# Kernel optimization log

Hardware: AMD Instinct MI355X
Metric: run time of the kernel (lower is better)

## Reference

```python
import jax, jax.numpy as jnp
import numpy as np

TWO_PI = 2.0 * np.pi
POW25_7 = 25.0 ** 7
M_RGB2XYZ = np.array([[0.4124564, 0.3575761, 0.1804375],
                      [0.2126729, 0.7151522, 0.072175],
                      [0.0193339, 0.119192, 0.9503041]], dtype=np.float32)
XYZ_REF = np.array([0.95047, 1.0, 1.08883], dtype=np.float32)


def rgb_to_lab(rgb):
    # rgb: [B, 3] in [0, 1]
    lin = jnp.where(rgb > 0.04045, ((rgb + 0.055) / 1.055) ** 2.4, rgb / 12.92)
    xyz = lin @ jnp.asarray(M_RGB2XYZ).T
    xyz_n = xyz / jnp.asarray(XYZ_REF)
    f = jnp.where(xyz_n > 0.008856, jnp.cbrt(xyz_n), 7.787 * xyz_n + 16.0 / 116.0)
    L = 116.0 * f[:, 1] - 16.0
    a = 500.0 * (f[:, 0] - f[:, 1])
    b = 200.0 * (f[:, 1] - f[:, 2])
    return L, a, b


def delta_e_2000(lab1, lab2):
    L1, a1, b1 = lab1
    L2, a2, b2 = lab2
    C1 = jnp.sqrt(a1 ** 2 + b1 ** 2)
    C2 = jnp.sqrt(a2 ** 2 + b2 ** 2)
    C_avg = (C1 + C2) / 2
    C_avg7 = C_avg ** 7
    G = 0.5 * (1 - jnp.sqrt(C_avg7 / (C_avg7 + POW25_7)))
    a1p = a1 * (1 + G)
    a2p = a2 * (1 + G)
    C1p = jnp.sqrt(a1p ** 2 + b1 ** 2)
    C2p = jnp.sqrt(a2p ** 2 + b2 ** 2)
    h1p = jnp.arctan2(b1, a1p) % TWO_PI
    h2p = jnp.arctan2(b2, a2p) % TWO_PI
    dL = L2 - L1
    dC = C2p - C1p
    dh = h2p - h1p
    dh = jnp.where(jnp.abs(dh) > np.pi,
                   jnp.where(h2p <= h1p, dh + TWO_PI, dh - TWO_PI), dh)
    dH = 2 * jnp.sqrt(C1p * C2p) * jnp.sin(dh / 2)
    L_avg = (L1 + L2) / 2
    Cp_avg = (C1p + C2p) / 2
    h_avg = jnp.where(jnp.abs(h1p - h2p) > np.pi,
                      (h1p + h2p + TWO_PI) / 2, (h1p + h2p) / 2)
    T = (1 - 0.17 * jnp.cos(h_avg - np.pi / 6)
         + 0.24 * jnp.cos(2 * h_avg)
         + 0.32 * jnp.cos(3 * h_avg + np.pi / 30)
         - 0.2 * jnp.cos(4 * h_avg - 7 * np.pi / 20))
    theta = 30 * jnp.exp(-(((h_avg * 180.0 / np.pi) - 275.0) / 25.0) ** 2)
    Cp_avg7 = Cp_avg ** 7
    RC = 2 * jnp.sqrt(Cp_avg7 / (Cp_avg7 + POW25_7))
    RT = -jnp.sin(2 * theta) * RC
    SL = 1 + 0.015 * (L_avg - 50) ** 2 / jnp.sqrt(20 + (L_avg - 50) ** 2)
    SC = 1 + 0.045 * Cp_avg
    SH = 1 + 0.015 * Cp_avg * T
    return jnp.sqrt((dL / SL) ** 2 + (dC / SC) ** 2 + (dH / SH) ** 2
                    + RT * (dC / SC) * (dH / SH))


def setup_inputs() -> dict:
    key = jax.random.key(0)
    k1, k2 = jax.random.split(key)
    B = 16777216
    pred = jax.random.uniform(k1, (B, 3), dtype=jnp.float32)
    target = jax.random.uniform(k2, (B, 3), dtype=jnp.float32)
    return {"pred": pred, "target": target}


def reference(pred, target):
    mse_loss = jnp.mean((pred - target) ** 2, axis=1)  # [B]
    de = delta_e_2000(rgb_to_lab(pred), rgb_to_lab(target))  # [B]
    # original detaches delta_e (computed on CPU numpy, written into a new tensor)
    combined = 0.2 * mse_loss + 0.8 * jax.lax.stop_gradient(de)
    return jnp.mean(combined)
```

## Files before the change

### kernel.cpp

```cpp
#include <hip/hip_runtime.h>
#include <math.h>

#define TPB 256
#define MAXBLOCKS 8192

typedef float v4f __attribute__((ext_vector_type(4)));

__device__ __forceinline__ float fsqrt_(float x){ return __builtin_amdgcn_sqrtf(x); }
__device__ __forceinline__ float frcp_ (float x){ return __builtin_amdgcn_rcpf(x); }
__device__ __forceinline__ float frsq_ (float x){ return __builtin_amdgcn_rsqf(x); }
__device__ __forceinline__ float flog2_(float x){ return __builtin_amdgcn_logf(x); }
__device__ __forceinline__ float fexp2_(float x){ return __builtin_amdgcn_exp2f(x); }
__device__ __forceinline__ float fsinr_(float x){ return __builtin_amdgcn_sinf(x); }

__device__ __forceinline__ v4f vs(float x){ return (v4f){x, x, x, x}; }

#define V4APPLY(fn, a) ((v4f){ fn((a).x), fn((a).y), fn((a).z), fn((a).w) })
__device__ __forceinline__ v4f vsqrt(v4f a){ return V4APPLY(fsqrt_, a); }
__device__ __forceinline__ v4f vrcp (v4f a){ return V4APPLY(frcp_ , a); }
__device__ __forceinline__ v4f vrsq (v4f a){ return V4APPLY(frsq_ , a); }
__device__ __forceinline__ v4f vlog2(v4f a){ return V4APPLY(flog2_, a); }
__device__ __forceinline__ v4f vexp2(v4f a){ return V4APPLY(fexp2_, a); }
__device__ __forceinline__ v4f vsinr(v4f a){ return V4APPLY(fsinr_, a); }

#if __has_builtin(__builtin_elementwise_fma)
__device__ __forceinline__ v4f vfma(v4f a, v4f b, v4f c){ return __builtin_elementwise_fma(a,b,c); }
#else
__device__ __forceinline__ v4f vfma(v4f a, v4f b, v4f c){ return a*b + c; }
#endif
__device__ __forceinline__ v4f vmax(v4f a, v4f b){ return __builtin_elementwise_max(a,b); }
__device__ __forceinline__ v4f vmin(v4f a, v4f b){ return __builtin_elementwise_min(a,b); }
__device__ __forceinline__ v4f vabs(v4f a){ return __builtin_elementwise_abs(a); }
__device__ __forceinline__ v4f vselgt(v4f x, float t, v4f a, v4f b){
    v4f r;
    r.x = x.x > t ? a.x : b.x;
    r.y = x.y > t ? a.y : b.y;
    r.z = x.z > t ? a.z : b.z;
    r.w = x.w > t ? a.w : b.w;
    return r;
}
__device__ __forceinline__ v4f vcopysign(v4f m, v4f s){
    v4f r;
    r.x = copysignf(m.x, s.x);
    r.y = copysignf(m.y, s.y);
    r.z = copysignf(m.z, s.z);
    r.w = copysignf(m.w, s.w);
    return r;
}

__device__ __forceinline__ v4f srgb_lin(v4f c){
    v4f t = (c + vs(0.055f)) * vs(1.0f/1.055f);
    v4f p = vexp2(vs(2.4f) * vlog2(t));
    return vselgt(c, 0.04045f, p, c * vs(1.0f/12.92f));
}
__device__ __forceinline__ v4f lab_f(v4f t){
    v4f cb = vexp2(vs(1.0f/3.0f) * vlog2(t));
    return vselgt(t, 0.008856f, cb, vfma(vs(7.787f), t, vs(16.0f/116.0f)));
}

__device__ __forceinline__ void rgb2lab(v4f r, v4f g, v4f b, v4f& L, v4f& A, v4f& Bv){
    v4f lr = srgb_lin(r), lg = srgb_lin(g), lb = srgb_lin(b);
    v4f xn = vfma(vs(0.4339499f), lr, vfma(vs(0.3762098f), lg, vs(0.1898414f)*lb));
    v4f yn = vfma(vs(0.2126729f), lr, vfma(vs(0.7151522f), lg, vs(0.0721750f)*lb));
    v4f zn = vfma(vs(0.0177566f), lr, vfma(vs(0.1094680f), lg, vs(0.8727720f)*lb));
    v4f fx = lab_f(xn), fy = lab_f(yn), fz = lab_f(zn);
    L  = vfma(vs(116.0f), fy, vs(-16.0f));
    A  = vs(500.0f) * (fx - fy);
    Bv = vs(200.0f) * (fy - fz);
}

__device__ __forceinline__ v4f vatan2_2pi(v4f y, v4f x){
    v4f ax = vabs(x), ay = vabs(y);
    v4f mx = vmax(ax, ay), mn = vmin(ax, ay);
    v4f t = mn * vrcp(vmax(mx, vs(1e-38f)));
    v4f s = t * t;
    v4f p = vs(-0.01172120f);
    p = vfma(p, s, vs( 0.05265332f));
    p = vfma(p, s, vs(-0.11643287f));
    p = vfma(p, s, vs( 0.19354346f));
    p = vfma(p, s, vs(-0.33262347f));
    p = vfma(p, s, vs( 0.99997726f));
    p = p * t;
    v4f r = vselgt(ay - ax, 0.0f, vs(1.57079632679f) - p, p);
    r = vselgt(vs(0.0f) - x, 0.0f, vs(3.14159265359f) - r, r);
    r = vselgt(vs(0.0f) - y, 0.0f, vs(6.28318530718f) - r, r);
    return r;
}

__device__ __forceinline__ v4f row_loss(v4f pr, v4f pg, v4f pb,
                                        v4f tr, v4f tg, v4f tb){
    const float P257 = 6103515625.0f;

    v4f dr = pr - tr, dg = pg - tg, db = pb - tb;
    v4f mse = (dr*dr + dg*dg + db*db) * vs(1.0f/3.0f);

    v4f L1, a1, b1, L2, a2, b2;
    rgb2lab(pr, pg, pb, L1, a1, b1);
    rgb2lab(tr, tg, tb, L2, a2, b2);

    v4f C1 = vsqrt(vfma(a1, a1, b1*b1));
    v4f C2 = vsqrt(vfma(a2, a2, b2*b2));
    v4f Cav = vs(0.5f) * (C1 + C2);
    v4f c2v = Cav*Cav;
    v4f c7 = c2v*c2v*c2v*Cav;
    v4f gs = vsqrt(c7 * vrcp(c7 + vs(P257)));
    v4f opG = vfma(vs(-0.5f), gs, vs(1.5f));
    v4f a1p = a1 * opG;
    v4f a2p = a2 * opG;
    v4f C1p = vsqrt(vfma(a1p, a1p, b1*b1));
    v4f C2p = vsqrt(vfma(a2p, a2p, b2*b2));

    v4f dL = L2 - L1;
    v4f dC = C2p - C1p;

    v4f prod  = C1p * C2p;
    v4f dot   = vfma(a1p, a2p, b1*b2);
    v4f cross = vfma(a1p, b2, vs(0.0f) - a2p*b1);
    v4f dH = vcopysign(vsqrt(vmax(vs(2.0f)*(prod - dot), vs(0.0f))), cross);

    v4f Lav  = vs(0.5f) * (L1 + L2);
    v4f Cpav = vs(0.5f) * (C1p + C2p);

    v4f vx = vfma(a1p, C2p, a2p*C1p);
    v4f vy = vfma(b1 , C2p, b2 *C1p);
    v4f hav = vatan2_2pi(vy, vx);
    v4f inv = vrsq(vmax(vfma(vx, vx, vy*vy), vs(1e-30f)));
    v4f ch = vx * inv, sh = vy * inv;

    v4f cos2 = vfma(vs(2.0f)*ch, ch, vs(-1.0f));
    v4f sin2 = vs(2.0f) * sh * ch;
    v4f cos3 = ch * vfma(vs(2.0f), cos2, vs(-1.0f));
    v4f sin3 = sh * vfma(vs(2.0f), cos2, vs( 1.0f));
    v4f cos4 = vfma(vs(2.0f)*cos2, cos2, vs(-1.0f));
    v4f sin4 = vs(2.0f) * sin2 * cos2;
    v4f T = vs(1.0f);
    T = vfma(vs(-0.147224319f), ch,   T);
    T = vfma(vs(-0.085f),       sh,   T);
    T = vfma(vs( 0.24f),        cos2, T);
    T = vfma(vs( 0.318247006f), cos3, T);
    T = vfma(vs(-0.033449109f), sin3, T);
    T = vfma(vs(-0.090798100f), cos4, T);
    T = vfma(vs(-0.178201305f), sin4, T);

    v4f u = vfma(hav, vs(2.29183118f), vs(-11.0f));
    v4f theta = vs(30.0f) * vexp2(vs(-1.44269504f) * (u*u));

    v4f cp2 = Cpav*Cpav;
    v4f cp7 = cp2*cp2*cp2*Cpav;
    v4f RC = vs(2.0f) * vsqrt(cp7 * vrcp(cp7 + vs(P257)));
    v4f RT = vs(0.0f) - vsinr(theta * vs(0.31830988618f)) * RC;

    v4f Lm = Lav - vs(50.0f);
    v4f Lm2 = Lm * Lm;
    v4f SL = vfma(vs(0.015f) * Lm2, vrsq(vs(20.0f) + Lm2), vs(1.0f));
    v4f SC = vfma(vs(0.045f), Cpav, vs(1.0f));
    v4f SH = vfma(vs(0.015f) * Cpav, T, vs(1.0f));

    v4f t1 = dL * vrcp(SL);
    v4f t2 = dC * vrcp(SC);
    v4f t3 = dH * vrcp(SH);
    v4f arg = vfma(t1, t1, vfma(t2, t2, vfma(t3, t3, RT*t2*t3)));
    v4f de = vsqrt(vmax(arg, vs(0.0f)));

    return vfma(vs(0.2f), mse, vs(0.8f) * de);
}

__global__ void __launch_bounds__(TPB)
de_main(const float* __restrict__ pred, const float* __restrict__ tgt,
        float* __restrict__ partials, int B){
    int nvec = B >> 2;
    int gid = blockIdx.x * TPB + threadIdx.x;
    int stride = gridDim.x * TPB;
    v4f acc4 = vs(0.0f);

    for (int i = gid; i < nvec; i += stride){
        const float4* p4 = (const float4*)pred + (size_t)i * 3;
        const float4* t4 = (const float4*)tgt  + (size_t)i * 3;
        float4 pA = p4[0], pB = p4[1], pC = p4[2];
        float4 tA = t4[0], tB = t4[1], tC = t4[2];
        v4f pr = (v4f){pA.x, pA.w, pB.z, pC.y};
        v4f pg = (v4f){pA.y, pB.x, pB.w, pC.z};
        v4f pb = (v4f){pA.z, pB.y, pC.x, pC.w};
        v4f qr = (v4f){tA.x, tA.w, tB.z, tC.y};
        v4f qg = (v4f){tA.y, tB.x, tB.w, tC.z};
        v4f qb = (v4f){tA.z, tB.y, tC.x, tC.w};
        acc4 += row_loss(pr, pg, pb, qr, qg, qb);
    }
    float acc = acc4.x + acc4.y + acc4.z + acc4.w;

    int r = (nvec << 2) + gid;
    if (r < B){
        v4f pr = vs(pred[(size_t)r*3]), pg = vs(pred[(size_t)r*3+1]), pb = vs(pred[(size_t)r*3+2]);
        v4f qr = vs(tgt [(size_t)r*3]), qg = vs(tgt [(size_t)r*3+1]), qb = vs(tgt [(size_t)r*3+2]);
        acc += row_loss(pr, pg, pb, qr, qg, qb).x;
    }

    __shared__ float sdata[TPB];
    sdata[threadIdx.x] = acc;
    __syncthreads();
    #pragma unroll
    for (int s = TPB/2; s > 0; s >>= 1){
        if (threadIdx.x < s) sdata[threadIdx.x] += sdata[threadIdx.x + s];
        __syncthreads();
    }
    if (threadIdx.x == 0) partials[blockIdx.x] = sdata[0];
}

__global__ void __launch_bounds__(TPB)
de_final(const float* __restrict__ partials, int n, float* __restrict__ out, double invB){
    __shared__ double sd[TPB];
    double acc = 0.0;
    for (int i = threadIdx.x; i < n; i += TPB) acc += (double)partials[i];
    sd[threadIdx.x] = acc;
    __syncthreads();
    #pragma unroll
    for (int s = TPB/2; s > 0; s >>= 1){
        if (threadIdx.x < s) sd[threadIdx.x] += sd[threadIdx.x + s];
        __syncthreads();
    }
    if (threadIdx.x == 0) out[0] = (float)(sd[0] * invB);
}

extern "C" void kernel_launch(void* const* d_in, const int* in_sizes, int n_in,
                              void* d_out, int out_size, void* d_ws, size_t ws_size,
                              hipStream_t stream){
    const float* pred = (const float*)d_in[0];
    const float* tgt  = (const float*)d_in[1];
    int B = in_sizes[0] / 3;

    int nvec = B >> 2;
    int blocks = (nvec + TPB - 1) / TPB;
    if (blocks > MAXBLOCKS) blocks = MAXBLOCKS;
    size_t wcap = ws_size / sizeof(float);
    if (wcap > 0 && (size_t)blocks > wcap) blocks = (int)wcap;
    if (blocks < 1) blocks = 1;

    float* partials = (float*)d_ws;
    de_main <<<blocks, TPB, 0, stream>>>(pred, tgt, partials, B);
    de_final<<<1, TPB, 0, stream>>>(partials, blocks, (float*)d_out, 1.0/(double)B);
}
```

Before: 417.1 us.

## Replace sRGB gamma and Lab cube-root transcendentals with shared-memory interpolated LUTs

Each block builds two 1032-entry shared-memory tables, one for the sRGB linearisation and one for the Lab f() cube root. Per-channel log2/exp2 pairs become linear interpolation between two LDS reads, with the XYZ matrix pre-scaled so its outputs index the table directly. The change also fuses sqrt(x/(x+k)) into one rsq, replaces three reciprocals with one, and lowers the block cap from 8192 to 2048 so fewer blocks pay the table build. The cost is interpolation error, random-index LDS bank conflicts, and out-of-bounds reads if any input falls outside [0,1].

After: 426.3 us. +2.2%, slower.

```diff
diff --git a/kernel.cpp b/kernel.cpp
--- a/kernel.cpp
+++ b/kernel.cpp
@@ -2,7 +2,8 @@
 #include <math.h>
 
 #define TPB 256
-#define MAXBLOCKS 8192
+#define NBLOCKS 2048
+#define LUTN 1032
 
 typedef float v4f __attribute__((ext_vector_type(4)));
 
@@ -12,6 +13,7 @@
 __device__ __forceinline__ float flog2_(float x){ return __builtin_amdgcn_logf(x); }
 __device__ __forceinline__ float fexp2_(float x){ return __builtin_amdgcn_exp2f(x); }
 __device__ __forceinline__ float fsinr_(float x){ return __builtin_amdgcn_sinf(x); }
+__device__ __forceinline__ float ffract_(float x){ return x - floorf(x); }
 
 __device__ __forceinline__ v4f vs(float x){ return (v4f){x, x, x, x}; }
 
@@ -19,8 +21,6 @@
 __device__ __forceinline__ v4f vsqrt(v4f a){ return V4APPLY(fsqrt_, a); }
 __device__ __forceinline__ v4f vrcp (v4f a){ return V4APPLY(frcp_ , a); }
 __device__ __forceinline__ v4f vrsq (v4f a){ return V4APPLY(frsq_ , a); }
-__device__ __forceinline__ v4f vlog2(v4f a){ return V4APPLY(flog2_, a); }
-__device__ __forceinline__ v4f vexp2(v4f a){ return V4APPLY(fexp2_, a); }
 __device__ __forceinline__ v4f vsinr(v4f a){ return V4APPLY(fsinr_, a); }
 
 #if __has_builtin(__builtin_elementwise_fma)
@@ -48,22 +48,25 @@
     return r;
 }
 
-__device__ __forceinline__ v4f srgb_lin(v4f c){
-    v4f t = (c + vs(0.055f)) * vs(1.0f/1.055f);
-    v4f p = vexp2(vs(2.4f) * vlog2(t));
-    return vselgt(c, 0.04045f, p, c * vs(1.0f/12.92f));
-}
-__device__ __forceinline__ v4f lab_f(v4f t){
-    v4f cb = vexp2(vs(1.0f/3.0f) * vlog2(t));
-    return vselgt(t, 0.008856f, cb, vfma(vs(7.787f), t, vs(16.0f/116.0f)));
-}
-
-__device__ __forceinline__ void rgb2lab(v4f r, v4f g, v4f b, v4f& L, v4f& A, v4f& Bv){
-    v4f lr = srgb_lin(r), lg = srgb_lin(g), lb = srgb_lin(b);
-    v4f xn = vfma(vs(0.4339499f), lr, vfma(vs(0.3762098f), lg, vs(0.1898414f)*lb));
-    v4f yn = vfma(vs(0.2126729f), lr, vfma(vs(0.7151522f), lg, vs(0.0721750f)*lb));
-    v4f zn = vfma(vs(0.0177566f), lr, vfma(vs(0.1094680f), lg, vs(0.8727720f)*lb));
-    v4f fx = lab_f(xn), fy = lab_f(yn), fz = lab_f(zn);
+__device__ __forceinline__ float lut1(const float* __restrict__ lut, float v){
+    int i = (int)v;
+    float f = ffract_(v);
+    float a = lut[i], b = lut[i+1];
+    return fmaf(f, b - a, a);
+}
+__device__ __forceinline__ v4f vlut(const float* __restrict__ lut, v4f v){
+    return (v4f){ lut1(lut, v.x), lut1(lut, v.y), lut1(lut, v.z), lut1(lut, v.w) };
+}
+
+__device__ __forceinline__ void rgb2lab(const float* __restrict__ lutS, const float* __restrict__ lutF,
+                                        v4f r, v4f g, v4f b, v4f& L, v4f& A, v4f& Bv){
+    v4f lr = vlut(lutS, r * vs(1024.0f));
+    v4f lg = vlut(lutS, g * vs(1024.0f));
+    v4f lb = vlut(lutS, b * vs(1024.0f));
+    v4f xi = vfma(vs(444.364687f), lr, vfma(vs(385.238808f), lg, vs(194.397593f)*lb));
+    v4f yi = vfma(vs(217.777050f), lr, vfma(vs(732.315853f), lg, vs( 73.907200f)*lb));
+    v4f zi = vfma(vs( 18.182738f), lr, vfma(vs(112.095395f), lg, vs(893.719306f)*lb));
+    v4f fx = vlut(lutF, xi), fy = vlut(lutF, yi), fz = vlut(lutF, zi);
     L  = vfma(vs(116.0f), fy, vs(-16.0f));
     A  = vs(500.0f) * (fx - fy);
     Bv = vs(200.0f) * (fy - fz);
@@ -87,7 +90,8 @@
     return r;
 }
 
-__device__ __forceinline__ v4f row_loss(v4f pr, v4f pg, v4f pb,
+__device__ __forceinline__ v4f row_loss(const float* __restrict__ lutS, const float* __restrict__ lutF,
+                                        v4f pr, v4f pg, v4f pb,
                                         v4f tr, v4f tg, v4f tb){
     const float P257 = 6103515625.0f;
 
@@ -95,15 +99,15 @@
     v4f mse = (dr*dr + dg*dg + db*db) * vs(1.0f/3.0f);
 
     v4f L1, a1, b1, L2, a2, b2;
-    rgb2lab(pr, pg, pb, L1, a1, b1);
-    rgb2lab(tr, tg, tb, L2, a2, b2);
+    rgb2lab(lutS, lutF, pr, pg, pb, L1, a1, b1);
+    rgb2lab(lutS, lutF, tr, tg, tb, L2, a2, b2);
 
     v4f C1 = vsqrt(vfma(a1, a1, b1*b1));
     v4f C2 = vsqrt(vfma(a2, a2, b2*b2));
     v4f Cav = vs(0.5f) * (C1 + C2);
     v4f c2v = Cav*Cav;
     v4f c7 = c2v*c2v*c2v*Cav;
-    v4f gs = vsqrt(c7 * vrcp(c7 + vs(P257)));
+    v4f gs = c7 * vrsq(vmax(c7*(c7 + vs(P257)), vs(1e-30f)));
     v4f opG = vfma(vs(-0.5f), gs, vs(1.5f));
     v4f a1p = a1 * opG;
     v4f a2p = a2 * opG;
@@ -143,11 +147,11 @@
     T = vfma(vs(-0.178201305f), sin4, T);
 
     v4f u = vfma(hav, vs(2.29183118f), vs(-11.0f));
-    v4f theta = vs(30.0f) * vexp2(vs(-1.44269504f) * (u*u));
+    v4f theta = vs(30.0f) * V4APPLY(fexp2_, (vs(-1.44269504f) * (u*u)));
 
     v4f cp2 = Cpav*Cpav;
     v4f cp7 = cp2*cp2*cp2*Cpav;
-    v4f RC = vs(2.0f) * vsqrt(cp7 * vrcp(cp7 + vs(P257)));
+    v4f RC = vs(2.0f) * (cp7 * vrsq(vmax(cp7*(cp7 + vs(P257)), vs(1e-30f))));
     v4f RT = vs(0.0f) - vsinr(theta * vs(0.31830988618f)) * RC;
 
     v4f Lm = Lav - vs(50.0f);
@@ -156,9 +160,13 @@
     v4f SC = vfma(vs(0.045f), Cpav, vs(1.0f));
     v4f SH = vfma(vs(0.015f) * Cpav, T, vs(1.0f));
 
-    v4f t1 = dL * vrcp(SL);
-    v4f t2 = dC * vrcp(SC);
-    v4f t3 = dH * vrcp(SH);
+    v4f SCSH = SC * SH;
+    v4f SLSH = SL * SH;
+    v4f SLSC = SL * SC;
+    v4f R = vrcp(SLSC * SH);
+    v4f t1 = dL * (SCSH * R);
+    v4f t2 = dC * (SLSH * R);
+    v4f t3 = dH * (SLSC * R);
     v4f arg = vfma(t1, t1, vfma(t2, t2, vfma(t3, t3, RT*t2*t3)));
     v4f de = vsqrt(vmax(arg, vs(0.0f)));
 
@@ -168,6 +176,17 @@
 __global__ void __launch_bounds__(TPB)
 de_main(const float* __restrict__ pred, const float* __restrict__ tgt,
         float* __restrict__ partials, int B){
+    __shared__ float lutS[LUTN];
+    __shared__ float lutF[LUTN];
+    for (int i = threadIdx.x; i < LUTN; i += TPB){
+        float c = (float)i * (1.0f/1024.0f);
+        float p = fexp2_(2.4f * flog2_((c + 0.055f) * (1.0f/1.055f)));
+        lutS[i] = (c > 0.04045f) ? p : c * (1.0f/12.92f);
+        float cb = fexp2_((1.0f/3.0f) * flog2_(fmaxf(c, 1e-20f)));
+        lutF[i] = (c > 0.008856f) ? cb : fmaf(7.787f, c, 16.0f/116.0f);
+    }
+    __syncthreads();
+
     int nvec = B >> 2;
     int gid = blockIdx.x * TPB + threadIdx.x;
     int stride = gridDim.x * TPB;
@@ -184,7 +203,7 @@
         v4f qr = (v4f){tA.x, tA.w, tB.z, tC.y};
         v4f qg = (v4f){tA.y, tB.x, tB.w, tC.z};
         v4f qb = (v4f){tA.z, tB.y, tC.x, tC.w};
-        acc4 += row_loss(pr, pg, pb, qr, qg, qb);
+        acc4 += row_loss(lutS, lutF, pr, pg, pb, qr, qg, qb);
     }
     float acc = acc4.x + acc4.y + acc4.z + acc4.w;
 
@@ -192,7 +211,7 @@
     if (r < B){
         v4f pr = vs(pred[(size_t)r*3]), pg = vs(pred[(size_t)r*3+1]), pb = vs(pred[(size_t)r*3+2]);
         v4f qr = vs(tgt [(size_t)r*3]), qg = vs(tgt [(size_t)r*3+1]), qb = vs(tgt [(size_t)r*3+2]);
-        acc += row_loss(pr, pg, pb, qr, qg, qb).x;
+        acc += row_loss(lutS, lutF, pr, pg, pb, qr, qg, qb).x;
     }
 
     __shared__ float sdata[TPB];
@@ -230,7 +249,7 @@
 
     int nvec = B >> 2;
     int blocks = (nvec + TPB - 1) / TPB;
-    if (blocks > MAXBLOCKS) blocks = MAXBLOCKS;
+    if (blocks > NBLOCKS) blocks = NBLOCKS;
     size_t wcap = ws_size / sizeof(float);
     if (wcap > 0 && (size_t)blocks > wcap) blocks = (int)wcap;
     if (blocks < 1) blocks = 1;
```
